# Kernel tuning notes

Measured on AMD Instinct MI355X. Metric: run time of the kernel, lower is better.

The kernel has to match this reference:

```python
import jax, jax.numpy as jnp
import numpy as np
from jax import lax

WS = 8            # window size
N = WS * WS       # tokens per window
NH = 8            # num heads
DIM = 256
HD = DIM // NH    # head dim


def _rel_tables():
    # continuous relative coords table, [1, 2*WS-1, 2*WS-1, 2]
    c = np.arange(-(WS - 1), WS, dtype=np.float32)
    table = np.stack(np.meshgrid(c, c, indexing='ij'), axis=-1)[None]
    table = table / (WS - 1) * 8.0
    table = np.sign(table) * np.log2(np.abs(table) + 1.0) / np.log2(8.0)
    # relative position index, [N, N] int
    coords = np.stack(np.meshgrid(np.arange(WS), np.arange(WS), indexing='ij'))
    cf = coords.reshape(2, -1)
    rel = (cf[:, :, None] - cf[:, None, :]).transpose(1, 2, 0)  # [N, N, 2]
    rel[..., 0] += WS - 1
    rel[..., 1] += WS - 1
    rel[..., 0] *= 2 * WS - 1
    idx = rel.sum(-1)
    return jnp.asarray(table, jnp.float32), jnp.asarray(idx, jnp.int32)


def setup_inputs() -> dict:
    key = jax.random.key(0)
    ks = jax.random.split(key, 12)
    s = 0.02
    return {
        'x': jax.random.normal(ks[0], (8, DIM, 128, 128), jnp.float32),
        'qkv_w': jax.random.normal(ks[1], (3 * DIM, DIM), jnp.float32) * s,
        'qkv_b': jax.random.normal(ks[2], (3 * DIM,), jnp.float32) * s,
        'proj_w': jax.random.normal(ks[3], (DIM, DIM), jnp.float32) * s,
        'proj_b': jax.random.normal(ks[4], (DIM,), jnp.float32) * s,
        'pe_w': jax.random.normal(ks[5], (DIM, 1, 3, 3), jnp.float32) * s,
        'pe_b': jax.random.normal(ks[6], (DIM,), jnp.float32) * s,
        'logit_scale': jnp.full((NH, 1, 1), np.log(10.0), jnp.float32),
        'cpb_w1': jax.random.normal(ks[7], (DIM, 2), jnp.float32) * s,
        'cpb_b1': jax.random.normal(ks[8], (DIM,), jnp.float32) * s,
        'cpb_w2': jax.random.normal(ks[9], (NH, DIM), jnp.float32) * s,
    }


def _conv1x1(x, w, b):
    # fused conv1x1 + eval-mode BN: [B,Ci,H,W] x [Co,Ci] -> [B,Co,H,W]
    return jnp.einsum('bchw,oc->bohw', x, w) + b[None, :, None, None]


def _window_partition(x):
    # [B,C,H,W] -> [B*nWh*nWw, N, C]; H,W divisible by WS (reflect pad no-op)
    B, C, H, W = x.shape
    x = x.reshape(B, C, H // WS, WS, W // WS, WS)
    x = x.transpose(0, 2, 4, 3, 5, 1)  # [B, nWh, nWw, ws, ws, C]
    return x.reshape(-1, N, C)


def _window_reverse(wins, B, H, W, C):
    # [B*nWh*nWw, N, C] -> [B, C, H, W]
    t = wins.reshape(B, H // WS, W // WS, WS, WS, C)
    t = t.transpose(0, 5, 1, 3, 2, 4)
    return t.reshape(B, C, H, W)


def reference(x, qkv_w, qkv_b, proj_w, proj_b, pe_w, pe_b,
              logit_scale, cpb_w1, cpb_b1, cpb_w2):
    B, C, H, W = x.shape
    table, idx = _rel_tables()

    qkv = _conv1x1(x, qkv_w, qkv_b)                      # [B, 3C, H, W]
    qkv_w_ = _window_partition(qkv)                      # [B_, N, 3C]
    B_ = qkv_w_.shape[0]
    qkv_w_ = qkv_w_.reshape(B_, N, NH, 3 * HD).transpose(0, 2, 1, 3)
    q, k, v = jnp.split(qkv_w_, 3, axis=-1)              # each [B_, NH, N, HD]

    qn = q / jnp.maximum(jnp.linalg.norm(q, axis=-1, keepdims=True), 1e-12)
    kn = k / jnp.maximum(jnp.linalg.norm(k, axis=-1, keepdims=True), 1e-12)
    attn = jnp.einsum('bhnd,bhmd->bhnm', qn, kn)         # cosine sim
    ls = jnp.exp(jnp.minimum(logit_scale, jnp.log(jnp.float32(100.0))))
    attn = attn * ls[None]                               # [B_, NH, N, N]

    # CPB MLP -> relative position bias gather
    h1 = jax.nn.relu(jnp.einsum('qtwc,dc->qtwd', table, cpb_w1) + cpb_b1)
    bias_table = jnp.einsum('qtwd,hd->qtwh', h1, cpb_w2).reshape(-1, NH)
    bias = bias_table[idx.reshape(-1)].reshape(N, N, NH).transpose(2, 0, 1)
    bias = 16.0 * jax.nn.sigmoid(bias)                   # [NH, N, N]

    attn = jax.nn.softmax(attn + bias[None], axis=-1)

    out = jnp.einsum('bhnm,bhmd->bhnd', attn, v)         # [B_, NH, N, HD]
    out = out.transpose(0, 2, 1, 3).reshape(B_, N, C)
    out_img = _window_reverse(out, B, H, W, C)           # [B, C, H, W]

    v_img = _window_reverse(v.transpose(0, 2, 1, 3).reshape(B_, N, C), B, H, W, C)
    pe = lax.conv_general_dilated(
        v_img, pe_w, (1, 1), 'SAME',
        dimension_numbers=('NCHW', 'OIHW', 'NCHW'),
        feature_group_count=C) + pe_b[None, :, None, None]

    return _conv1x1(out_img + pe, proj_w, proj_b)
```

## Files before the change

### kernel.cpp

```cpp
#include <hip/hip_runtime.h>

typedef unsigned short u16;
typedef unsigned int u32;
typedef short bf16x8 __attribute__((ext_vector_type(8)));
typedef float f32x4 __attribute__((ext_vector_type(4)));
typedef unsigned short u16x8 __attribute__((ext_vector_type(8)));
typedef unsigned short u16x4 __attribute__((ext_vector_type(4)));

#define DEVFN static __device__ __forceinline__

DEVFN u16 f2b(float f) {
    u32 u = __builtin_bit_cast(u32, f);
    u += 0x7FFFu + ((u >> 16) & 1u);
    return (u16)(u >> 16);
}
DEVFN float b2f(u16 h) {
    u32 u = ((u32)h) << 16;
    return __builtin_bit_cast(float, u);
}

typedef const __attribute__((address_space(1))) unsigned int glb_u32;
typedef __attribute__((address_space(3))) unsigned int lds_u32;
DEVFN void gload_lds16(const u16* g, u16* l) {
    __builtin_amdgcn_global_load_lds((glb_u32*)g, (lds_u32*)l, 16, 0, 0);
}

__global__ void k_prep(const float* __restrict__ qkvw, const float* __restrict__ pjw,
                       u16* __restrict__ qkvwb, u16* __restrict__ pjwb) {
    int id = blockIdx.x * 256 + threadIdx.x;
    if (id < 196608) qkvwb[id] = f2b(qkvw[id]);
    if (id < 65536)  pjwb[id]  = f2b(pjw[id]);
}

__global__ void k_cpb(const float* __restrict__ w1, const float* __restrict__ b1,
                      const float* __restrict__ w2, float* __restrict__ bt) {
    int p = threadIdx.x;
    if (p >= 225) return;
    int d0 = p / 15, d1 = p % 15;
    float v0 = (float)(d0 - 7) * (8.0f / 7.0f);
    float v1 = (float)(d1 - 7) * (8.0f / 7.0f);
    float t0 = copysignf(log2f(fabsf(v0) + 1.0f) * (1.0f / 3.0f), v0);
    float t1 = copysignf(log2f(fabsf(v1) + 1.0f) * (1.0f / 3.0f), v1);
    float s[8] = {0.f, 0.f, 0.f, 0.f, 0.f, 0.f, 0.f, 0.f};
    for (int d = 0; d < 256; ++d) {
        float h = t0 * w1[2 * d] + t1 * w1[2 * d + 1] + b1[d];
        h = fmaxf(h, 0.0f);
        #pragma unroll
        for (int hh = 0; hh < 8; ++hh) s[hh] += h * w2[hh * 256 + d];
    }
    #pragma unroll
    for (int hh = 0; hh < 8; ++hh) bt[p * 8 + hh] = s[hh];
}

__global__ void k_bias(const float* __restrict__ bt, float* __restrict__ biasT) {
    int id = blockIdx.x * 256 + threadIdx.x;
    int kq = id >> 6, q = id & 63;
    int d0 = (q >> 3) - (kq >> 3) + 7;
    int d1 = (q & 7) - (kq & 7) + 7;
    int p = d0 * 15 + d1;
    #pragma unroll
    for (int h = 0; h < 8; ++h)
        biasT[h * 4096 + id] = 16.0f / (1.0f + expf(-bt[p * 8 + h]));
}

__global__ __launch_bounds__(256) void k_xcvt(const float* __restrict__ x,
                                              u16* __restrict__ xt) {
    const int bid = blockIdx.x;
    const int xcd = bid & 7;
    const int i = bid >> 3;
    const int rowblk = xcd * 128 + (i >> 2);
    const int c = i & 3;
    const int tid = threadIdx.x;
    const int g = tid & 7;
    const int tseg = tid >> 3;
    const int tok0 = tseg * 4;
    const float* src = x + ((size_t)(rowblk >> 7) * 256 + c * 64 + g * 8) * 16384
                         + (rowblk & 127) * 128 + tok0;
    float4 v[8];
    #pragma unroll
    for (int j = 0; j < 8; ++j)
        v[j] = *(const float4*)(src + (size_t)j * 16384);
    u16x8 o0, o1, o2, o3;
    #pragma unroll
    for (int j = 0; j < 8; ++j) {
        o0[j] = f2b(v[j].x);
        o1[j] = f2b(v[j].y);
        o2[j] = f2b(v[j].z);
        o3[j] = f2b(v[j].w);
    }
    const int s0 = g ^ ((tseg ^ (tok0 + 0)) & 7);
    const int s1 = g ^ ((tseg ^ (tok0 + 1)) & 7);
    const int s2 = g ^ ((tseg ^ (tok0 + 2)) & 7);
    const int s3 = g ^ ((tseg ^ (tok0 + 3)) & 7);
    u16* dst = xt + ((size_t)rowblk * 4 + c) * 8192;
    *(u16x8*)&dst[(tok0 + 0) * 64 + (s0 << 3)] = o0;
    *(u16x8*)&dst[(tok0 + 1) * 64 + (s1 << 3)] = o1;
    *(u16x8*)&dst[(tok0 + 2) * 64 + (s2 << 3)] = o2;
    *(u16x8*)&dst[(tok0 + 3) * 64 + (s3 << 3)] = o3;
}

__global__ __launch_bounds__(256, 3) void k_qkv(
    const u16* __restrict__ xt, const u16* __restrict__ qkvw,
    const float* __restrict__ qkvb,
    u16* __restrict__ gq, u16* __restrict__ gk, u16* __restrict__ wv_g) {
    __shared__ __align__(16) u16 Xs[2][8192];

    const int bid = blockIdx.x;
    const int xcd = bid & 7;
    const int idx = bid >> 3;
    const int ny = idx % 6;
    const int rowblk = xcd * 128 + idx / 6;
    const int b = rowblk >> 7, row = rowblk & 127;
    const int which = ny >> 1, half = ny & 1;

    const int tid = threadIdx.x;
    const int wave = tid >> 6, l = tid & 63, col = l & 15, quad = l >> 4;
    const int th = wave >> 1;
    const int oq = wave & 1;
    const int obase = half * 128 + oq * 64;

    int orow[4];
    #pragma unroll
    for (int nt = 0; nt < 4; ++nt) {
        const int oo = obase + nt * 16 + col;
        orow[nt] = (oo >> 5) * 96 + which * 32 + (oo & 31);
    }

    f32x4 acc[4][4];
    #pragma unroll
    for (int i = 0; i < 4; ++i)
        #pragma unroll
        for (int j = 0; j < 4; ++j) acc[i][j] = f32x4{0.f, 0.f, 0.f, 0.f};

    const u16* xtb = xt + (size_t)rowblk * 32768;

    auto stage = [&](int c, int buf) {
        const u16* src = xtb + c * 8192 + wave * 2048 + l * 8;
        u16* dst = &Xs[buf][wave * 2048];
        #pragma unroll
        for (int i = 0; i < 4; ++i)
            gload_lds16(src + i * 512, dst + i * 512);
    };
    auto loadW = [&](int c, bf16x8* bw) {
        #pragma unroll
        for (int kk = 0; kk < 2; ++kk)
            #pragma unroll
            for (int nt = 0; nt < 4; ++nt)
                bw[kk * 4 + nt] = *(const bf16x8*)&qkvw[(size_t)orow[nt] * 256 +
                                                        c * 64 + kk * 32 + quad * 8];
    };
    auto gemm = [&](int buf, const bf16x8* bw) {
        #pragma unroll
        for (int kk = 0; kk < 2; ++kk) {
            const int lchunk = kk * 4 + quad;
            bf16x8 af[4];
            #pragma unroll
            for (int mt = 0; mt < 4; ++mt) {
                const int tok = th * 64 + mt * 16 + col;
                const int slot = lchunk ^ (((tok >> 2) ^ tok) & 7);
                af[mt] = *(const bf16x8*)&Xs[buf][tok * 64 + (slot << 3)];
            }
            #pragma unroll
            for (int nt = 0; nt < 4; ++nt)
                #pragma unroll
                for (int mt = 0; mt < 4; ++mt)
                    acc[nt][mt] = __builtin_amdgcn_mfma_f32_16x16x32_bf16(
                        bw[kk * 4 + nt], af[mt], acc[nt][mt], 0, 0, 0);
        }
    };

    bf16x8 bwA[8], bwB[8];
    stage(0, 0);
    loadW(0, bwA);
    __syncthreads();
    #pragma unroll
    for (int c = 0; c < 4; ++c) {
        if (c < 3) {
            stage(c + 1, (c + 1) & 1);
            loadW(c + 1, (c & 1) ? bwA : bwB);
        }
        gemm(c & 1, (c & 1) ? bwB : bwA);
        __syncthreads();
    }

    const int hA = obase >> 5;
    f32x4 bqv[4];
    #pragma unroll
    for (int nt = 0; nt < 4; ++nt) {
        const int oo = obase + nt * 16 + quad * 4;
        bqv[nt] = *(const f32x4*)&qkvb[(oo >> 5) * 96 + which * 32 + (oo & 31)];
    }
    #pragma unroll
    for (int mt = 0; mt < 4; ++mt) {
        const int tok = th * 64 + mt * 16 + col;
        const int win = b * 256 + (row >> 3) * 16 + (tok >> 3);
        const int tk = (row & 7) * 8 + (tok & 7);
        float v[4][4];
        #pragma unroll
        for (int nt = 0; nt < 4; ++nt)
            #pragma unroll
            for (int r = 0; r < 4; ++r)
                v[nt][r] = acc[nt][mt][r] + bqv[nt][r];
        if (which < 2) {
            float sA = 0.f, sB = 0.f;
            #pragma unroll
            for (int r = 0; r < 4; ++r) {
                sA += v[0][r] * v[0][r] + v[1][r] * v[1][r];
                sB += v[2][r] * v[2][r] + v[3][r] * v[3][r];
            }
            sA += __shfl_xor(sA, 16, 64);
            sA += __shfl_xor(sA, 32, 64);
            sB += __shfl_xor(sB, 16, 64);
            sB += __shfl_xor(sB, 32, 64);
            const float iA = 1.0f / fmaxf(sqrtf(sA), 1e-12f);
            const float iB = 1.0f / fmaxf(sqrtf(sB), 1e-12f);
            #pragma unroll
            for (int r = 0; r < 4; ++r) {
                v[0][r] *= iA; v[1][r] *= iA;
                v[2][r] *= iB; v[3][r] *= iB;
            }
        }
        #pragma unroll
        for (int nt = 0; nt < 4; ++nt) {
            u16x4 ov;
            #pragma unroll
            for (int r = 0; r < 4; ++r) ov[r] = f2b(v[nt][r]);
            if (which == 2) {
                *(u16x4*)&wv_g[((size_t)win * 64 + tk) * 256 + obase + nt * 16 + quad * 4] = ov;
            } else {
                u16* G = (which == 0) ? gq : gk;
                const int h = hA + (nt >> 1);
                const int d = (nt & 1) * 16 + quad * 4;
                *(u16x4*)&G[((size_t)(win * 8 + h) * 64 + tk) * 32 + d] = ov;
            }
        }
    }
}

__global__ __launch_bounds__(256, 3) void k_attn3(
    const u16* __restrict__ gq, const u16* __restrict__ gk,
    const u16* __restrict__ wv_g,
    const float* __restrict__ lsc, const float* __restrict__ biasT,
    u16* __restrict__ wout_g) {
    __shared__ __align__(16) u16 scr[4][2048];

    const int tid = threadIdx.x;
    const int wave = tid >> 6, l = tid & 63, col = l & 15, quad = l >> 4;
    const int bid = blockIdx.x;
    const int xcd = bid & 7;
    const int jl = (bid >> 3) * 4 + wave;
    const int h = jl >> 8;
    const int win = xcd * 256 + (jl & 255);
    u16* const v_t = scr[wave];

    u16x8 sv[4];
    #pragma unroll
    for (int it = 0; it < 4; ++it) {
        const int idx = it * 64 + l;
        const int tok = idx & 63, dblk = idx >> 6;
        sv[it] = *(const u16x8*)&wv_g[((size_t)win * 64 + tok) * 256 + h * 32 + dblk * 8];
    }
    const u16* const qbp = gq + (size_t)(win * 8 + h) * 2048;
    const u16* const kbp = gk + (size_t)(win * 8 + h) * 2048;
    bf16x8 ak[4], bq[4];
    #pragma unroll
    for (int mt = 0; mt < 4; ++mt)
        ak[mt] = *(const bf16x8*)&kbp[(mt * 16 + col) * 32 + quad * 8];
    #pragma unroll
    for (int nt = 0; nt < 4; ++nt)
        bq[nt] = *(const bf16x8*)&qbp[(nt * 16 + col) * 32 + quad * 8];

    #pragma unroll
    for (int it = 0; it < 4; ++it) {
        const int idx = it * 64 + l;
        const int tok = idx & 63, dblk = idx >> 6;
        const int g = (tok >> 5) * 4 + ((tok >> 2) & 3);
        const int jj = ((tok >> 4) & 1) * 4 + (tok & 3);
        #pragma unroll
        for (int j = 0; j < 8; ++j) {
            const int d = dblk * 8 + j;
            v_t[d * 64 + (((g ^ (d & 7)) << 3) | jj)] = sv[it][j];
        }
    }

    const f32x4 zero4 = {0.f, 0.f, 0.f, 0.f};
    f32x4 sacc[4][4];
    #pragma unroll
    for (int mt = 0; mt < 4; ++mt)
        #pragma unroll
        for (int nt = 0; nt < 4; ++nt)
            sacc[mt][nt] = __builtin_amdgcn_mfma_f32_16x16x32_bf16(ak[mt], bq[nt], zero4, 0, 0, 0);

    const float ls = expf(fminf(lsc[h], 4.6051701859880914f));
    const float* bT = biasT + h * 4096;
    #pragma unroll
    for (int nt = 0; nt < 4; ++nt) {
        const int q = nt * 16 + col;
        float v[4][4];
        float mx = -1e30f;
        #pragma unroll
        for (int mt = 0; mt < 4; ++mt)
            #pragma unroll
            for (int r = 0; r < 4; ++r) {
                v[mt][r] = sacc[mt][nt][r] * ls + bT[(mt * 16 + quad * 4 + r) * 64 + q];
                mx = fmaxf(mx, v[mt][r]);
            }
        mx = fmaxf(mx, __shfl_xor(mx, 16, 64));
        mx = fmaxf(mx, __shfl_xor(mx, 32, 64));
        float s = 0.f;
        #pragma unroll
        for (int mt = 0; mt < 4; ++mt)
            #pragma unroll
            for (int r = 0; r < 4; ++r) {
                v[mt][r] = expf(v[mt][r] - mx);
                s += v[mt][r];
            }
        s += __shfl_xor(s, 16, 64);
        s += __shfl_xor(s, 32, 64);
        const float inv = 1.0f / s;
        #pragma unroll
        for (int mt = 0; mt < 4; ++mt)
            #pragma unroll
            for (int r = 0; r < 4; ++r)
                sacc[mt][nt][r] = v[mt][r] * inv;
    }

    f32x4 oacc[2][4];
    #pragma unroll
    for (int i = 0; i < 2; ++i)
        #pragma unroll
        for (int j = 0; j < 4; ++j) oacc[i][j] = zero4;
    #pragma unroll
    for (int kk = 0; kk < 2; ++kk) {
        bf16x8 av[2];
        #pragma unroll
        for (int dt = 0; dt < 2; ++dt) {
            const int d = dt * 16 + col;
            av[dt] = *(const bf16x8*)&v_t[d * 64 + (((kk * 4 + quad) ^ (d & 7)) << 3)];
        }
        #pragma unroll
        for (int nt = 0; nt < 4; ++nt) {
            union { u16x8 u; bf16x8 b; } pk;
            #pragma unroll
            for (int j = 0; j < 4; ++j) {
                pk.u[j]     = f2b(sacc[kk * 2][nt][j]);
                pk.u[j + 4] = f2b(sacc[kk * 2 + 1][nt][j]);
            }
            #pragma unroll
            for (int dt = 0; dt < 2; ++dt)
                oacc[dt][nt] = __builtin_amdgcn_mfma_f32_16x16x32_bf16(
                    av[dt], pk.b, oacc[dt][nt], 0, 0, 0);
        }
    }
    #pragma unroll
    for (int dt = 0; dt < 2; ++dt)
        #pragma unroll
        for (int qt = 0; qt < 4; ++qt) {
            const int t = qt * 16 + col;
            u16x4 ov;
            #pragma unroll
            for (int r = 0; r < 4; ++r) ov[r] = f2b(oacc[dt][qt][r]);
            *(u16x4*)&wout_g[((size_t)win * 64 + t) * 256 + h * 32 + dt * 16 + quad * 4] = ov;
        }
}

__global__ __launch_bounds__(256, 4) void k_proj(
    const u16* __restrict__ wout_g, const u16* __restrict__ wv_g,
    const float* __restrict__ pe_w, const float* __restrict__ pe_b,
    const u16* __restrict__ pjw, const float* __restrict__ pjb,
    float* __restrict__ out) {
    __shared__ __align__(16) u16 y_s[64 * 256];
    const int bid0 = blockIdx.x;
    const int win = (bid0 & 7) * 256 + (bid0 >> 3);
    const int b = win >> 8;
    const int h0 = ((win >> 4) & 15) * 8;
    const int w0 = (win & 15) * 8;
    const int tid = threadIdx.x;
    const int cg = tid & 31, ch = cg * 8;
    const int psub = tid >> 5;

    float pw[9][8];
    #pragma unroll
    for (int j = 0; j < 8; ++j)
        #pragma unroll
        for (int k = 0; k < 9; ++k) pw[k][j] = pe_w[(ch + j) * 9 + k];
    float pb[8];
    #pragma unroll
    for (int j = 0; j < 8; ++j) pb[j] = pe_b[ch + j];

    for (int it = 0; it < 8; ++it) {
        const int p = it * 8 + psub;
        const int gh = h0 + (p >> 3), gw = w0 + (p & 7);
        float a[8];
        {
            const bf16x8 ov = *(const bf16x8*)&wout_g[((size_t)win * 64 + p) * 256 + ch];
            #pragma unroll
            for (int j = 0; j < 8; ++j) a[j] = b2f((u16)ov[j]) + pb[j];
        }
        #pragma unroll
        for (int dy = -1; dy <= 1; ++dy)
            #pragma unroll
            for (int dx = -1; dx <= 1; ++dx) {
                const int hh = gh + dy, ww2 = gw + dx;
                if (hh < 0 || hh >= 128 || ww2 < 0 || ww2 >= 128) continue;
                const int nwin = b * 256 + (hh >> 3) * 16 + (ww2 >> 3);
                const int ntk = (hh & 7) * 8 + (ww2 & 7);
                const bf16x8 vv = *(const bf16x8*)&wv_g[((size_t)nwin * 64 + ntk) * 256 + ch];
                const int k = (dy + 1) * 3 + (dx + 1);
                #pragma unroll
                for (int j = 0; j < 8; ++j) a[j] += b2f((u16)vv[j]) * pw[k][j];
            }
        u16x8 tmp;
        #pragma unroll
        for (int j = 0; j < 8; ++j) tmp[j] = f2b(a[j]);
        *(u16x8*)&y_s[p * 256 + (((ch >> 3) ^ (p & 7)) << 3)] = tmp;
    }
    __syncthreads();

    const int wave = tid >> 6, l = tid & 63;
    const int col = l & 15, quad = l >> 4;
    const f32x4 zero4 = {0.f, 0.f, 0.f, 0.f};
    f32x4 macc[4][4];
    #pragma unroll
    for (int pt = 0; pt < 4; ++pt)
        #pragma unroll
        for (int ot = 0; ot < 4; ++ot) macc[pt][ot] = zero4;
    const int ob = wave * 64;
    for (int kk = 0; kk < 8; ++kk) {
        const int cb = kk * 32 + quad * 8;
        bf16x8 aw[4], by[4];
        #pragma unroll
        for (int ot = 0; ot < 4; ++ot)
            aw[ot] = *(const bf16x8*)&pjw[(size_t)(ob + ot * 16 + col) * 256 + cb];
        #pragma unroll
        for (int pt = 0; pt < 4; ++pt) {
            const int p = pt * 16 + col;
            by[pt] = *(const bf16x8*)&y_s[p * 256 + (((cb >> 3) ^ (p & 7)) << 3)];
        }
        #pragma unroll
        for (int pt = 0; pt < 4; ++pt)
            #pragma unroll
            for (int ot = 0; ot < 4; ++ot)
                macc[pt][ot] = __builtin_amdgcn_mfma_f32_16x16x32_bf16(
                    by[pt], aw[ot], macc[pt][ot], 0, 0, 0);
    }
    #pragma unroll
    for (int ot = 0; ot < 4; ++ot) {
        const int o = ob + ot * 16 + col;
        const float pbv = pjb[o];
        #pragma unroll
        for (int pt = 0; pt < 4; ++pt) {
            const int p0 = pt * 16 + quad * 4;
            float4 ov;
            ov.x = macc[pt][ot][0] + pbv;
            ov.y = macc[pt][ot][1] + pbv;
            ov.z = macc[pt][ot][2] + pbv;
            ov.w = macc[pt][ot][3] + pbv;
            *(float4*)&out[((size_t)(b * 256 + o)) * 16384 +
                           (h0 + (p0 >> 3)) * 128 + w0 + (p0 & 7)] = ov;
        }
    }
}

extern "C" void kernel_launch(void* const* d_in, const int* in_sizes, int n_in,
                              void* d_out, int out_size, void* d_ws, size_t ws_size,
                              hipStream_t stream) {
    const float* x    = (const float*)d_in[0];
    const float* qkvw = (const float*)d_in[1];
    const float* qkvb = (const float*)d_in[2];
    const float* pjw  = (const float*)d_in[3];
    const float* pjb  = (const float*)d_in[4];
    const float* pew  = (const float*)d_in[5];
    const float* peb  = (const float*)d_in[6];
    const float* lsc  = (const float*)d_in[7];
    const float* w1   = (const float*)d_in[8];
    const float* b1   = (const float*)d_in[9];
    const float* w2   = (const float*)d_in[10];

    char* ws = (char*)d_ws;
    u16* wv_b    = (u16*)(ws);
    u16* wout_b  = (u16*)(ws + (64ull << 20));
    u16* qkvwb   = (u16*)(ws + (128ull << 20));
    u16* pjwb    = (u16*)(ws + (128ull << 20) + 393216);
    float* biasT = (float*)(ws + (128ull << 20) + 393216 + 131072);
    float* bt    = (float*)(ws + (128ull << 20) + 393216 + 262144);

    u16* xt = wout_b;
    u16* gq = (u16*)d_out;
    u16* gk = gq + 33554432u;

    hipLaunchKernelGGL(k_prep, dim3(768), dim3(256), 0, stream, qkvw, pjw, qkvwb, pjwb);
    hipLaunchKernelGGL(k_cpb,  dim3(1),   dim3(256), 0, stream, w1, b1, w2, bt);
    hipLaunchKernelGGL(k_bias, dim3(16),  dim3(256), 0, stream, bt, biasT);
    hipLaunchKernelGGL(k_xcvt, dim3(4096), dim3(256), 0, stream, x, xt);
    hipLaunchKernelGGL(k_qkv,  dim3(6144), dim3(256), 0, stream,
                       xt, qkvwb, qkvb, gq, gk, wv_b);
    hipLaunchKernelGGL(k_attn3, dim3(4096), dim3(256), 0, stream,
                       gq, gk, wv_b, lsc, biasT, wout_b);
    hipLaunchKernelGGL(k_proj, dim3(2048), dim3(256), 0, stream,
                       wout_b, wv_b, pew, peb, pjwb, pjb, (float*)d_out);
}
```

Measured before the change: 388.1 us.

## Process two row blocks per QKV block with continuous cross-tile prefetch

Each k_qkv block now computes two consecutive row blocks, so the grid is halved. The staging loop runs across eight K-chunks, which lets the prefetch of the second row block's X tile and weights overlap the first block's GEMM and epilogue. This is meant to cut per-block prologue, pipeline fill and launch overhead. In exchange there is less block-level parallelism and more code inside the loop, which may raise register pressure.

```diff
diff --git a/kernel.cpp b/kernel.cpp
--- a/kernel.cpp
+++ b/kernel.cpp
@@ -109,8 +109,7 @@
     const int xcd = bid & 7;
     const int idx = bid >> 3;
     const int ny = idx % 6;
-    const int rowblk = xcd * 128 + idx / 6;
-    const int b = rowblk >> 7, row = rowblk & 127;
+    const int rowblk0 = xcd * 128 + (idx / 6) * 2;
     const int which = ny >> 1, half = ny & 1;
 
     const int tid = threadIdx.x;
@@ -132,11 +131,10 @@
         #pragma unroll
         for (int j = 0; j < 4; ++j) acc[i][j] = f32x4{0.f, 0.f, 0.f, 0.f};
 
-    const u16* xtb = xt + (size_t)rowblk * 32768;
-
-    auto stage = [&](int c, int buf) {
-        const u16* src = xtb + c * 8192 + wave * 2048 + l * 8;
-        u16* dst = &Xs[buf][wave * 2048];
+    auto stage8 = [&](int g) {
+        const u16* src = xt + (size_t)(rowblk0 + (g >> 2)) * 32768 +
+                         (g & 3) * 8192 + wave * 2048 + l * 8;
+        u16* dst = &Xs[g & 1][wave * 2048];
         #pragma unroll
         for (int i = 0; i < 4; ++i)
             gload_lds16(src + i * 512, dst + i * 512);
@@ -168,73 +166,83 @@
                         bw[kk * 4 + nt], af[mt], acc[nt][mt], 0, 0, 0);
         }
     };
+    const int hA = obase >> 5;
+    auto epilogue = [&](int rowblk) {
+        const int b = rowblk >> 7, row = rowblk & 127;
+        f32x4 bqv[4];
+        #pragma unroll
+        for (int nt = 0; nt < 4; ++nt) {
+            const int oo = obase + nt * 16 + quad * 4;
+            bqv[nt] = *(const f32x4*)&qkvb[(oo >> 5) * 96 + which * 32 + (oo & 31)];
+        }
+        #pragma unroll
+        for (int mt = 0; mt < 4; ++mt) {
+            const int tok = th * 64 + mt * 16 + col;
+            const int win = b * 256 + (row >> 3) * 16 + (tok >> 3);
+            const int tk = (row & 7) * 8 + (tok & 7);
+            float v[4][4];
+            #pragma unroll
+            for (int nt = 0; nt < 4; ++nt)
+                #pragma unroll
+                for (int r = 0; r < 4; ++r)
+                    v[nt][r] = acc[nt][mt][r] + bqv[nt][r];
+            if (which < 2) {
+                float sA = 0.f, sB = 0.f;
+                #pragma unroll
+                for (int r = 0; r < 4; ++r) {
+                    sA += v[0][r] * v[0][r] + v[1][r] * v[1][r];
+                    sB += v[2][r] * v[2][r] + v[3][r] * v[3][r];
+                }
+                sA += __shfl_xor(sA, 16, 64);
+                sA += __shfl_xor(sA, 32, 64);
+                sB += __shfl_xor(sB, 16, 64);
+                sB += __shfl_xor(sB, 32, 64);
+                const float iA = 1.0f / fmaxf(sqrtf(sA), 1e-12f);
+                const float iB = 1.0f / fmaxf(sqrtf(sB), 1e-12f);
+                #pragma unroll
+                for (int r = 0; r < 4; ++r) {
+                    v[0][r] *= iA; v[1][r] *= iA;
+                    v[2][r] *= iB; v[3][r] *= iB;
+                }
+            }
+            #pragma unroll
+            for (int nt = 0; nt < 4; ++nt) {
+                u16x4 ov;
+                #pragma unroll
+                for (int r = 0; r < 4; ++r) ov[r] = f2b(v[nt][r]);
+                if (which == 2) {
+                    *(u16x4*)&wv_g[((size_t)win * 64 + tk) * 256 + obase + nt * 16 + quad * 4] = ov;
+                } else {
+                    u16* G = (which == 0) ? gq : gk;
+                    const int h = hA + (nt >> 1);
+                    const int d = (nt & 1) * 16 + quad * 4;
+                    *(u16x4*)&G[((size_t)(win * 8 + h) * 64 + tk) * 32 + d] = ov;
+                }
+            }
+        }
+    };
 
     bf16x8 bwA[8], bwB[8];
-    stage(0, 0);
+    stage8(0);
     loadW(0, bwA);
     __syncthreads();
     #pragma unroll
-    for (int c = 0; c < 4; ++c) {
-        if (c < 3) {
-            stage(c + 1, (c + 1) & 1);
-            loadW(c + 1, (c & 1) ? bwA : bwB);
-        }
-        gemm(c & 1, (c & 1) ? bwB : bwA);
-        __syncthreads();
-    }
-
-    const int hA = obase >> 5;
-    f32x4 bqv[4];
-    #pragma unroll
-    for (int nt = 0; nt < 4; ++nt) {
-        const int oo = obase + nt * 16 + quad * 4;
-        bqv[nt] = *(const f32x4*)&qkvb[(oo >> 5) * 96 + which * 32 + (oo & 31)];
-    }
-    #pragma unroll
-    for (int mt = 0; mt < 4; ++mt) {
-        const int tok = th * 64 + mt * 16 + col;
-        const int win = b * 256 + (row >> 3) * 16 + (tok >> 3);
-        const int tk = (row & 7) * 8 + (tok & 7);
-        float v[4][4];
-        #pragma unroll
-        for (int nt = 0; nt < 4; ++nt)
-            #pragma unroll
-            for (int r = 0; r < 4; ++r)
-                v[nt][r] = acc[nt][mt][r] + bqv[nt][r];
-        if (which < 2) {
-            float sA = 0.f, sB = 0.f;
-            #pragma unroll
-            for (int r = 0; r < 4; ++r) {
-                sA += v[0][r] * v[0][r] + v[1][r] * v[1][r];
-                sB += v[2][r] * v[2][r] + v[3][r] * v[3][r];
-            }
-            sA += __shfl_xor(sA, 16, 64);
-            sA += __shfl_xor(sA, 32, 64);
-            sB += __shfl_xor(sB, 16, 64);
-            sB += __shfl_xor(sB, 32, 64);
-            const float iA = 1.0f / fmaxf(sqrtf(sA), 1e-12f);
-            const float iB = 1.0f / fmaxf(sqrtf(sB), 1e-12f);
-            #pragma unroll
-            for (int r = 0; r < 4; ++r) {
-                v[0][r] *= iA; v[1][r] *= iA;
-                v[2][r] *= iB; v[3][r] *= iB;
-            }
-        }
-        #pragma unroll
-        for (int nt = 0; nt < 4; ++nt) {
-            u16x4 ov;
-            #pragma unroll
-            for (int r = 0; r < 4; ++r) ov[r] = f2b(v[nt][r]);
-            if (which == 2) {
-                *(u16x4*)&wv_g[((size_t)win * 64 + tk) * 256 + obase + nt * 16 + quad * 4] = ov;
-            } else {
-                u16* G = (which == 0) ? gq : gk;
-                const int h = hA + (nt >> 1);
-                const int d = (nt & 1) * 16 + quad * 4;
-                *(u16x4*)&G[((size_t)(win * 8 + h) * 64 + tk) * 32 + d] = ov;
-            }
-        }
-    }
+    for (int g = 0; g < 8; ++g) {
+        if (g < 7) {
+            stage8(g + 1);
+            loadW((g + 1) & 3, (g & 1) ? bwA : bwB);
+        }
+        gemm(g & 1, (g & 1) ? bwB : bwA);
+        if (g == 3) {
+            epilogue(rowblk0);
+            #pragma unroll
+            for (int i = 0; i < 4; ++i)
+                #pragma unroll
+                for (int j = 0; j < 4; ++j) acc[i][j] = f32x4{0.f, 0.f, 0.f, 0.f};
+        }
+        if (g < 7) __syncthreads();
+    }
+    epilogue(rowblk0 + 1);
 }
 
 __global__ __launch_bounds__(256, 3) void k_attn3(
@@ -493,7 +501,7 @@
     hipLaunchKernelGGL(k_cpb,  dim3(1),   dim3(256), 0, stream, w1, b1, w2, bt);
     hipLaunchKernelGGL(k_bias, dim3(16),  dim3(256), 0, stream, bt, biasT);
     hipLaunchKernelGGL(k_xcvt, dim3(4096), dim3(256), 0, stream, x, xt);
-    hipLaunchKernelGGL(k_qkv,  dim3(6144), dim3(256), 0, stream,
+    hipLaunchKernelGGL(k_qkv,  dim3(3072), dim3(256), 0, stream,
                        xt, qkvwb, qkvb, gq, gk, wv_b);
     hipLaunchKernelGGL(k_attn3, dim3(4096), dim3(256), 0, stream,
                        gq, gk, wv_b, lsc, biasT, wout_b);
```

Measured after the change: 432.8 us. +11.5%, slower.
